# Performance work log

Hardware: AMD Instinct MI355X
Metric: run time of the kernel (lower is better)

Reference implementation:

```python
import jax, jax.numpy as jnp
import numpy as np

B, T, F = 512, 512, 16
UNITS = [64, 32, 32, 32]
VOCAB, EDIM = 1281, 4


def setup_inputs() -> dict:
    key = jax.random.key(0)
    ks = jax.random.split(key, 32)
    x = jax.random.normal(ks[0], (B, T, F), jnp.float32)
    # column 1 holds integer org ids (stored as float, as in the TF model)
    ids = jax.random.randint(ks[1], (B, T), 0, VOCAB).astype(jnp.float32)
    x = x.at[:, :, 1].set(ids)
    d = {"input_tensor": x,
         "emb": jax.random.normal(ks[2], (VOCAB, EDIM), jnp.float32) * 0.05}
    din = 1 + (F - 2) + EDIM  # 18
    i = 3
    for l, u in enumerate(UNITS):
        d[f"k{l}"] = jax.random.normal(ks[i], (din, 3 * u), jnp.float32) * 0.1; i += 1
        d[f"r{l}"] = jax.random.normal(ks[i], (u, 3 * u), jnp.float32) * 0.1; i += 1
        d[f"bi{l}"] = jnp.zeros((3 * u,), jnp.float32)
        d[f"bh{l}"] = jnp.zeros((3 * u,), jnp.float32)
        din = u
    u = UNITS[-1]
    d["w1"] = jax.random.normal(ks[i], (u, u), jnp.float32) * 0.1; i += 1
    d["b1"] = jnp.zeros((u,), jnp.float32)
    d["w2"] = jax.random.normal(ks[i], (u, u), jnp.float32) * 0.1; i += 1
    d["b2"] = jnp.zeros((u,), jnp.float32)
    d["v"] = jax.random.normal(ks[i], (u, 1), jnp.float32) * 0.1; i += 1
    d["bv"] = jnp.zeros((1,), jnp.float32)
    d["wd"] = jax.random.normal(ks[i], (u, 2), jnp.float32) * 0.1; i += 1
    d["bd"] = jnp.zeros((2,), jnp.float32)
    return d


def _gru(h, xp, rk, bh):
    # Keras GRUCell (reset_after=True). xp = x @ kernel + input_bias, [B, 3u]
    hp = h @ rk + bh
    xz, xr, xh = jnp.split(xp, 3, axis=-1)
    hz, hr, hhp = jnp.split(hp, 3, axis=-1)
    z = jax.nn.sigmoid(xz + hz)
    r = jax.nn.sigmoid(xr + hr)
    hh = jnp.tanh(xh + r * hhp)
    return z * h + (1.0 - z) * hh


def _forward(input_tensor, emb, k0, r0, bi0, bh0, k1, r1, bi1, bh1,
             k2, r2, bi2, bh2, k3, r3, bi3, bh3,
             w1, b1, w2, b2, v, bv, wd, bd):
    f0 = input_tensor[:, :, :1]                      # [B,T,1]
    ids = input_tensor[:, :, 1].astype(jnp.int32)    # [B,T]
    rest = input_tensor[:, :, 2:]                    # [B,T,F-2]
    e = emb[ids]                                     # [B,T,4]
    inp = jnp.concatenate([f0, rest, e], axis=2)     # [B,T,din]

    # precompute layer-0 input projection as one big GEMM
    xp0 = inp @ k0 + bi0                             # [B,T,3*64]
    bsz = inp.shape[0]
    init = tuple(jnp.zeros((bsz, u), inp.dtype) for u in UNITS)

    def step(carry, xp_t):
        h0, h1, h2, h3 = carry
        h0 = _gru(h0, xp_t, r0, bh0)
        h1 = _gru(h1, h0 @ k1 + bi1, r1, bh1)
        h2 = _gru(h2, h1 @ k2 + bi2, r2, bh2)
        h3 = _gru(h3, h2 @ k3 + bi3, r3, bh3)
        return (h0, h1, h2, h3), h3

    (_, _, _, hT), seq = jax.lax.scan(step, init, jnp.swapaxes(xp0, 0, 1))
    outputs = jnp.swapaxes(seq, 0, 1)                # [B,T,32] (last-layer sequence)

    # Bahdanau attention: query = final state of last layer
    score = jnp.tanh(outputs @ w1 + b1 + (hT @ w2 + b2)[:, None, :]) @ v + bv  # [B,T,1]
    attn = jax.nn.softmax(score, axis=1)
    ctx = jnp.sum(attn * outputs, axis=1)            # [B,32]
    return jax.nn.softmax(ctx @ wd + bd, axis=-1)    # [B,2]


def reference(input_tensor, emb, k0, r0, bi0, bh0, k1, r1, bi1, bh1,
              k2, r2, bi2, bh2, k3, r3, bi3, bh3,
              w1, b1, w2, b2, v, bv, wd, bd):
    return _forward(input_tensor, emb, k0, r0, bi0, bh0, k1, r1, bi1, bh1,
                    k2, r2, bi2, bh2, k3, r3, bi3, bh3,
                    w1, b1, w2, b2, v, bv, wd, bd)
```

## Files before the change

kernel.cpp:

```cpp
#include <hip/hip_runtime.h>

#define TLEN 512
#define FIN 16

__device__ __forceinline__ float sigm(float x) { return 1.0f / (1.0f + __expf(-x)); }
__device__ __forceinline__ float tanh_f(float x) {
  x = fminf(fmaxf(x, -15.0f), 15.0f);
  float e = __expf(2.0f * x);
  return (e - 1.0f) / (e + 1.0f);
}

__device__ __forceinline__ float gru_fin(float own_main, float own_xh, float own_hhp,
                                         int role, float hold) {
  const float oth_main = __shfl_xor(own_main, 1);
  const float xh  = own_xh  + __shfl_xor(own_xh, 1);
  const float hhp = own_hhp + __shfl_xor(own_hhp, 1);
  const float sz = role ? oth_main : own_main;
  const float sr = role ? own_main : oth_main;
  const float z = sigm(sz);
  const float r = sigm(sr);
  const float hh = tanh_f(xh + r * hhp);
  return z * hold + (1.f - z) * hh;
}

__global__ __launch_bounds__(256, 1)
void rnn_pipe2(const float* __restrict__ x, const float* __restrict__ emb,
               const float* __restrict__ k0, const float* __restrict__ r0,
               const float* __restrict__ bi0, const float* __restrict__ bh0,
               const float* __restrict__ k1, const float* __restrict__ r1,
               const float* __restrict__ bi1, const float* __restrict__ bh1,
               const float* __restrict__ k2, const float* __restrict__ r2,
               const float* __restrict__ bi2, const float* __restrict__ bh2,
               const float* __restrict__ k3, const float* __restrict__ r3,
               const float* __restrict__ bi3, const float* __restrict__ bh3,
               const float* __restrict__ w1, const float* __restrict__ b1,
               const float* __restrict__ w2, const float* __restrict__ b2,
               const float* __restrict__ vv, const float* __restrict__ bv,
               const float* __restrict__ wd, const float* __restrict__ bd,
               float* __restrict__ out, float* __restrict__ obuf)
{
  __shared__ __align__(16) float s_h0[2][64][2];
  __shared__ __align__(16) float s_h1[2][32][2];
  __shared__ __align__(16) float s_h2[2][32][2];
  __shared__ __align__(16) float s_h3[2][32][2];
  __shared__ __align__(16) float s_inp[2][20][2];
  __shared__ __align__(16) float s_emb[2][TLEN][4];
  __shared__ __align__(16) float s_pA[2][64][2];
  __shared__ __align__(16) float s_pAh[2][64][2];
  __shared__ __align__(16) float e_w1[1024];
  __shared__ __align__(16) float e_sc[1024];
  __shared__ float e_hw2[64], e_b1[32], e_v[32], e_ctx[64];

  const int tid  = threadIdx.x;
  const int wid  = tid >> 6;
  const int lane = tid & 63;
  const int g    = lane >> 1;
  const int role = lane & 1;
  const int bb0  = blockIdx.x * 2;

  float Wa[96], Wb[48], Wc[48];
  float bm = 0.f, bxh = 0.f, bhh = 0.f;
  float cbm = 0.f, cbxh = 0.f, cbhh = 0.f;
  float rxP = 0.f;

  if (wid <= 1) {
    const int u  = wid * 32 + g;
    const int cm = role ? 64 + u : u;
    #pragma unroll
    for (int j = 0; j < 19; ++j) Wa[j] = k0[j*192 + cm];
    Wa[19] = 0.f;
    #pragma unroll
    for (int j = 0; j < 64; ++j) Wa[20+j] = r0[j*192 + cm];
    #pragma unroll
    for (int jj = 0; jj < 10; ++jj) {
      const int row = role*10 + jj;
      Wb[jj] = (row < 19) ? k0[row*192 + 128 + u] : 0.f;
    }
    #pragma unroll
    for (int jj = 0; jj < 32; ++jj) Wb[10+jj] = r0[(role*32+jj)*192 + 128 + u];
    bm  = bi0[cm] + bh0[cm];
    bxh = role ? 0.f : bi0[128+u];
    bhh = role ? bh0[128+u] : 0.f;
  }
  if (wid == 0) {
    const int cma = role ? 32 + g : g;
    #pragma unroll
    for (int j = 0; j < 32; ++j) Wc[j] = k3[j*96 + cma];
    #pragma unroll
    for (int jj = 0; jj < 16; ++jj) Wc[32+jj] = k3[(role*16+jj)*96 + 64 + g];
  }
  if (wid == 2) {
    const int cm = role ? 32 + g : g;
    #pragma unroll
    for (int j = 0; j < 64; ++j) Wa[j] = k1[j*96 + cm];
    #pragma unroll
    for (int j = 0; j < 32; ++j) Wa[64+j] = r1[j*96 + cm];
    #pragma unroll
    for (int jj = 0; jj < 32; ++jj) Wb[jj] = k1[(role*32+jj)*96 + 64 + g];
    #pragma unroll
    for (int jj = 0; jj < 16; ++jj) Wb[32+jj] = r1[(role*16+jj)*96 + 64 + g];
    bm  = bi1[cm] + bh1[cm];
    bxh = role ? 0.f : bi1[64+g];
    bhh = role ? bh1[64+g] : 0.f;
  }
  if (wid == 3) {
    const int cm = role ? 32 + g : g;
    #pragma unroll
    for (int j = 0; j < 32; ++j) Wa[j] = k2[j*96 + cm];
    #pragma unroll
    for (int j = 0; j < 32; ++j) Wa[32+j] = r2[j*96 + cm];
    #pragma unroll
    for (int jj = 0; jj < 16; ++jj) Wb[jj] = k2[(role*16+jj)*96 + 64 + g];
    #pragma unroll
    for (int jj = 0; jj < 16; ++jj) Wb[16+jj] = r2[(role*16+jj)*96 + 64 + g];
    bm  = bi2[cm] + bh2[cm];
    bxh = role ? 0.f : bi2[64+g];
    bhh = role ? bh2[64+g] : 0.f;
    #pragma unroll
    for (int j = 0; j < 32; ++j) Wc[j] = r3[j*96 + cm];
    #pragma unroll
    for (int jj = 0; jj < 16; ++jj) Wc[32+jj] = r3[(role*16+jj)*96 + 64 + g];
    cbm  = bi3[cm] + bh3[cm];
    cbxh = bi3[64+g];
    cbhh = bh3[64+g];
  }

  ((float*)s_h0)[tid] = 0.f;
  if (tid < 128) {
    ((float*)s_h1)[tid] = 0.f;
    ((float*)s_h2)[tid] = 0.f;
    ((float*)s_h3)[tid] = 0.f;
  }
  if (tid < 80) ((float*)s_inp)[tid] = 0.f;

  for (int q = tid; q < 2*TLEN; q += 256) {
    const int b2 = q >> 9, t2 = q & 511;
    const int id = (int)x[((size_t)(bb0+b2)*TLEN + t2)*FIN + 1];
    *(float4*)&s_emb[b2][t2][0] = *(const float4*)&emb[id*4];
  }
  if (wid == 1 && lane < 32) {
    const int b2 = lane >> 4, f = lane & 15;
    rxP = x[((size_t)(bb0+b2)*TLEN + 1)*FIN + f];
  }
  __syncthreads();
  if (tid < 32) {
    const int b2 = tid >> 4, f = tid & 15;
    const float v = x[((size_t)(bb0+b2)*TLEN + 0)*FIN + f];
    if (f == 0) s_inp[0][0][b2] = v;
    else if (f >= 2) s_inp[0][f-1][b2] = v;
    if (f < 4) s_inp[0][15+f][b2] = s_emb[b2][0][f];
  }

  for (int i = 0; i < 516; ++i) {
    __syncthreads();
    const int wp = i & 1;
    const int rp = wp ^ 1;

    if (wid <= 1) {
      if (i < 512) {
        const int u = wid*32 + g;
        float a0A = bm, a0B = bm, a1A = 0.f, a1B = 0.f;
        #pragma unroll
        for (int j = 0; j < 20; j += 2) {
          const float4 q = *(const float4*)&s_inp[wp][j][0];
          a0A += Wa[j]*q.x;   a0B += Wa[j]*q.y;
          a1A += Wa[j+1]*q.z; a1B += Wa[j+1]*q.w;
        }
        #pragma unroll
        for (int j = 0; j < 64; j += 2) {
          const float4 q = *(const float4*)&s_h0[rp][j][0];
          a0A += Wa[20+j]*q.x; a0B += Wa[20+j]*q.y;
          a1A += Wa[21+j]*q.z; a1B += Wa[21+j]*q.w;
        }
        float xqA = bxh, xqB = bxh;
        #pragma unroll
        for (int jj = 0; jj < 10; ++jj) {
          const float2 d = *(const float2*)&s_inp[wp][role*10+jj][0];
          xqA += Wb[jj]*d.x; xqB += Wb[jj]*d.y;
        }
        float p0A = bhh, p0B = bhh, p1A = 0.f, p1B = 0.f;
        #pragma unroll
        for (int jj = 0; jj < 32; jj += 2) {
          const float4 q = *(const float4*)&s_h0[rp][role*32+jj][0];
          p0A += Wb[10+jj]*q.x; p0B += Wb[10+jj]*q.y;
          p1A += Wb[11+jj]*q.z; p1B += Wb[11+jj]*q.w;
        }
        const float holdA = s_h0[rp][u][0];
        const float holdB = s_h0[rp][u][1];
        const float hnA = gru_fin(a0A+a1A, xqA, p0A+p1A, role, holdA);
        const float hnB = gru_fin(a0B+a1B, xqB, p0B+p1B, role, holdB);
        if (!role) { s_h0[wp][u][0] = hnA; s_h0[wp][u][1] = hnB; }
      }
      if (wid == 0) {
        if (i >= 3 && i <= 514) {
          float q0A=0.f,q0B=0.f,q1A=0.f,q1B=0.f;
          #pragma unroll
          for (int j = 0; j < 32; j += 2) {
            const float4 q = *(const float4*)&s_h2[rp][j][0];
            q0A += Wc[j]*q.x;   q0B += Wc[j]*q.y;
            q1A += Wc[j+1]*q.z; q1B += Wc[j+1]*q.w;
          }
          float phA=0.f, phB=0.f, ph1A=0.f, ph1B=0.f;
          #pragma unroll
          for (int jj = 0; jj < 16; jj += 2) {
            const float4 q = *(const float4*)&s_h2[rp][role*16+jj][0];
            phA  += Wc[32+jj]*q.x; phB  += Wc[32+jj]*q.y;
            ph1A += Wc[33+jj]*q.z; ph1B += Wc[33+jj]*q.w;
          }
          s_pA[wp][lane][0]  = q0A+q1A;  s_pA[wp][lane][1]  = q0B+q1B;
          s_pAh[wp][lane][0] = phA+ph1A; s_pAh[wp][lane][1] = phB+ph1B;
        }
      } else {
        if (lane < 32) {
          const int b2 = lane >> 4, f = lane & 15;
          if (i + 1 <= 511) {
            const int slot = (i+1)&1;
            const float v = rxP;
            if (f == 0) s_inp[slot][0][b2] = v;
            else if (f >= 2) s_inp[slot][f-1][b2] = v;
            if (f < 4) s_inp[slot][15+f][b2] = s_emb[b2][i+1][f];
          }
          if (i + 2 <= 511) rxP = x[((size_t)(bb0+b2)*TLEN + (i+2))*FIN + f];
        }
      }
    } else if (wid == 2) {
      if (i >= 1 && i <= 512) {
        float a0A = bm, a0B = bm, a1A=0.f, a1B=0.f;
        #pragma unroll
        for (int j = 0; j < 64; j += 2) {
          const float4 q = *(const float4*)&s_h0[rp][j][0];
          a0A += Wa[j]*q.x;   a0B += Wa[j]*q.y;
          a1A += Wa[j+1]*q.z; a1B += Wa[j+1]*q.w;
        }
        #pragma unroll
        for (int j = 0; j < 32; j += 2) {
          const float4 q = *(const float4*)&s_h1[rp][j][0];
          a0A += Wa[64+j]*q.x; a0B += Wa[64+j]*q.y;
          a1A += Wa[65+j]*q.z; a1B += Wa[65+j]*q.w;
        }
        float x0A = bxh, x0B = bxh, x1A = 0.f, x1B = 0.f;
        #pragma unroll
        for (int jj = 0; jj < 32; jj += 2) {
          const float4 q = *(const float4*)&s_h0[rp][role*32+jj][0];
          x0A += Wb[jj]*q.x;   x0B += Wb[jj]*q.y;
          x1A += Wb[jj+1]*q.z; x1B += Wb[jj+1]*q.w;
        }
        float p0A = bhh, p0B = bhh, p1A = 0.f, p1B = 0.f;
        #pragma unroll
        for (int jj = 0; jj < 16; jj += 2) {
          const float4 q = *(const float4*)&s_h1[rp][role*16+jj][0];
          p0A += Wb[32+jj]*q.x; p0B += Wb[32+jj]*q.y;
          p1A += Wb[33+jj]*q.z; p1B += Wb[33+jj]*q.w;
        }
        const float holdA = s_h1[rp][g][0];
        const float holdB = s_h1[rp][g][1];
        const float hnA = gru_fin(a0A+a1A, x0A+x1A, p0A+p1A, role, holdA);
        const float hnB = gru_fin(a0B+a1B, x0B+x1B, p0B+p1B, role, holdB);
        if (!role) { s_h1[wp][g][0] = hnA; s_h1[wp][g][1] = hnB; }
      }
    } else {
      if (i >= 2 && i <= 513) {
        float a0A = bm, a0B = bm, a1A=0.f, a1B=0.f;
        #pragma unroll
        for (int j = 0; j < 32; j += 2) {
          const float4 q = *(const float4*)&s_h1[rp][j][0];
          a0A += Wa[j]*q.x;   a0B += Wa[j]*q.y;
          a1A += Wa[j+1]*q.z; a1B += Wa[j+1]*q.w;
        }
        #pragma unroll
        for (int j = 0; j < 32; j += 2) {
          const float4 q = *(const float4*)&s_h2[rp][j][0];
          a0A += Wa[32+j]*q.x; a0B += Wa[32+j]*q.y;
          a1A += Wa[33+j]*q.z; a1B += Wa[33+j]*q.w;
        }
        float x0A = bxh, x0B = bxh, x1A = 0.f, x1B = 0.f;
        #pragma unroll
        for (int jj = 0; jj < 16; jj += 2) {
          const float4 q = *(const float4*)&s_h1[rp][role*16+jj][0];
          x0A += Wb[jj]*q.x;   x0B += Wb[jj]*q.y;
          x1A += Wb[jj+1]*q.z; x1B += Wb[jj+1]*q.w;
        }
        float p0A = bhh, p0B = bhh, p1A = 0.f, p1B = 0.f;
        #pragma unroll
        for (int jj = 0; jj < 16; jj += 2) {
          const float4 q = *(const float4*)&s_h2[rp][role*16+jj][0];
          p0A += Wb[16+jj]*q.x; p0B += Wb[16+jj]*q.y;
          p1A += Wb[17+jj]*q.z; p1B += Wb[17+jj]*q.w;
        }
        const float holdA = s_h2[rp][g][0];
        const float holdB = s_h2[rp][g][1];
        const float hnA = gru_fin(a0A+a1A, x0A+x1A, p0A+p1A, role, holdA);
        const float hnB = gru_fin(a0B+a1B, x0B+x1B, p0B+p1B, role, holdB);
        if (!role) { s_h2[wp][g][0] = hnA; s_h2[wp][g][1] = hnB; }
      }
      if (i >= 4) {
        float q0A=0.f,q0B=0.f,q1A=0.f,q1B=0.f;
        #pragma unroll
        for (int jj = 0; jj < 32; jj += 2) {
          const float4 q = *(const float4*)&s_h3[rp][jj][0];
          q0A += Wc[jj]*q.x;   q0B += Wc[jj]*q.y;
          q1A += Wc[jj+1]*q.z; q1B += Wc[jj+1]*q.w;
        }
        float ph0A=0.f, ph0B=0.f, ph1A=0.f, ph1B=0.f;
        #pragma unroll
        for (int jj = 0; jj < 16; jj += 2) {
          const float4 q = *(const float4*)&s_h3[rp][role*16+jj][0];
          ph0A += Wc[32+jj]*q.x; ph0B += Wc[32+jj]*q.y;
          ph1A += Wc[33+jj]*q.z; ph1B += Wc[33+jj]*q.w;
        }
        const float mainA = s_pA[rp][lane][0] + q0A + q1A + cbm;
        const float mainB = s_pA[rp][lane][1] + q0B + q1B + cbm;
        const float xhA_own = s_pAh[rp][lane][0];
        const float xhB_own = s_pAh[rp][lane][1];
        const float phA_own = ph0A + ph1A;
        const float phB_own = ph0B + ph1B;

        const float othA = __shfl_xor(mainA, 1);
        const float othB = __shfl_xor(mainB, 1);
        const float xhA = xhA_own + __shfl_xor(xhA_own, 1) + cbxh;
        const float xhB = xhB_own + __shfl_xor(xhB_own, 1) + cbxh;
        const float hhpA = phA_own + __shfl_xor(phA_own, 1) + cbhh;
        const float hhpB = phB_own + __shfl_xor(phB_own, 1) + cbhh;

        const float szA = role ? othA : mainA;
        const float srA = role ? mainA : othA;
        const float szB = role ? othB : mainB;
        const float srB = role ? mainB : othB;
        const float zA = sigm(szA), rA = sigm(srA);
        const float zB = sigm(szB), rB = sigm(srB);
        const float hhA = tanh_f(xhA + rA*hhpA);
        const float hhB = tanh_f(xhB + rB*hhpB);
        const float hnA = zA*s_h3[rp][g][0] + (1.f-zA)*hhA;
        const float hnB = zB*s_h3[rp][g][1] + (1.f-zB)*hhB;
        if (!role) {
          s_h3[wp][g][0] = hnA;
          s_h3[wp][g][1] = hnB;
          obuf[((size_t)(bb0+0)*TLEN + (i-4))*32 + g] = hnA;
          obuf[((size_t)(bb0+1)*TLEN + (i-4))*32 + g] = hnB;
        }
      }
    }
  }
  __syncthreads();

  for (int kk = tid; kk < 1024; kk += 256) e_w1[kk] = w1[kk];
  if (tid < 32) { e_b1[tid] = b1[tid]; e_v[tid] = vv[tid]; }
  if (tid >= 64 && tid < 128) {
    const int u = tid & 31, bb = (tid - 64) >> 5;
    float s = b2[u];
    #pragma unroll
    for (int j = 0; j < 32; ++j) s += s_h3[1][j][bb] * w2[j*32 + u];
    e_hw2[bb*32 + u] = s;
  }
  __syncthreads();

  #pragma unroll
  for (int c = 0; c < 4; ++c) {
    const int idx = c*256 + tid;
    const int bb = idx >> 9, t2 = idx & 511;
    const float* row = obuf + ((size_t)(bb0+bb)*TLEN + t2)*32;
    float rr[32];
    #pragma unroll
    for (int j = 0; j < 32; j += 4) {
      const float4 r4 = *(const float4*)&row[j];
      rr[j]=r4.x; rr[j+1]=r4.y; rr[j+2]=r4.z; rr[j+3]=r4.w;
    }
    float sc = 0.f;
    for (int u = 0; u < 32; ++u) {
      float qv = e_b1[u] + e_hw2[bb*32 + u];
      #pragma unroll
      for (int j = 0; j < 32; ++j) qv += rr[j]*e_w1[j*32+u];
      sc += tanh_f(qv)*e_v[u];
    }
    e_sc[idx] = sc;
  }
  __syncthreads();

  {
    if (wid < 2) {
      const int bb = wid;
      float sv[8]; float m = -1e30f;
      #pragma unroll
      for (int k = 0; k < 8; ++k) { sv[k] = e_sc[bb*512 + lane + 64*k]; m = fmaxf(m, sv[k]); }
      #pragma unroll
      for (int off = 32; off > 0; off >>= 1) m = fmaxf(m, __shfl_xor(m, off));
      float ss = 0.f;
      #pragma unroll
      for (int k = 0; k < 8; ++k) { sv[k] = __expf(sv[k]-m); ss += sv[k]; }
      #pragma unroll
      for (int off = 32; off > 0; off >>= 1) ss += __shfl_xor(ss, off);
      const float inv = 1.f/ss;
      #pragma unroll
      for (int k = 0; k < 8; ++k) e_sc[bb*512 + lane + 64*k] = sv[k]*inv;
    }
  }
  __syncthreads();

  if (tid < 64) {
    const int u = tid & 31, bb = tid >> 5;
    float acc = 0.f;
    const float* orow = obuf + (size_t)(bb0+bb)*TLEN*32 + u;
    const float* prow = e_sc + bb*512;
    #pragma unroll 4
    for (int t2 = 0; t2 < 512; ++t2) acc += prow[t2]*orow[(size_t)t2*32];
    e_ctx[bb*32 + u] = acc;
  }
  __syncthreads();

  if (tid < 2) {
    const int bb = tid;
    float l0 = bd[0], l1 = bd[1];
    #pragma unroll
    for (int u = 0; u < 32; ++u) {
      const float cv = e_ctx[bb*32 + u];
      l0 += cv*wd[u*2]; l1 += cv*wd[u*2+1];
    }
    const float mm = fmaxf(l0, l1);
    const float ex0 = __expf(l0-mm), ex1 = __expf(l1-mm);
    const float den = ex0 + ex1;
    out[(bb0+bb)*2 + 0] = ex0/den;
    out[(bb0+bb)*2 + 1] = ex1/den;
  }
}

extern "C" void kernel_launch(void* const* d_in, const int* in_sizes, int n_in,
                              void* d_out, int out_size, void* d_ws, size_t ws_size,
                              hipStream_t stream) {
  const float* x   = (const float*)d_in[0];
  const float* emb = (const float*)d_in[1];
  const float* k0  = (const float*)d_in[2];
  const float* r0  = (const float*)d_in[3];
  const float* bi0 = (const float*)d_in[4];
  const float* bh0 = (const float*)d_in[5];
  const float* k1  = (const float*)d_in[6];
  const float* r1  = (const float*)d_in[7];
  const float* bi1 = (const float*)d_in[8];
  const float* bh1 = (const float*)d_in[9];
  const float* k2  = (const float*)d_in[10];
  const float* r2  = (const float*)d_in[11];
  const float* bi2 = (const float*)d_in[12];
  const float* bh2 = (const float*)d_in[13];
  const float* k3  = (const float*)d_in[14];
  const float* r3  = (const float*)d_in[15];
  const float* bi3 = (const float*)d_in[16];
  const float* bh3 = (const float*)d_in[17];
  const float* w1  = (const float*)d_in[18];
  const float* b1  = (const float*)d_in[19];
  const float* w2  = (const float*)d_in[20];
  const float* b2  = (const float*)d_in[21];
  const float* v   = (const float*)d_in[22];
  const float* bv  = (const float*)d_in[23];
  const float* wd  = (const float*)d_in[24];
  const float* bd  = (const float*)d_in[25];

  float* out  = (float*)d_out;
  float* obuf = (float*)d_ws;

  rnn_pipe2<<<dim3(256), dim3(256), 0, stream>>>(
      x, emb, k0, r0, bi0, bh0, k1, r1, bi1, bh1,
      k2, r2, bi2, bh2, k3, r3, bi3, bh3,
      w1, b1, w2, b2, v, bv, wd, bd, out, obuf);
}
```

Measured before the change: 1.156 ms.

## Preload all timestep inputs into LDS and batch output stores via staging buffer

Instead of a warp prefetching one timestep of input and embedding per iteration into a double-buffered slot, the kernel now loads the whole 512-step input sequence (features plus gathered embedding) into shared memory up front with vectorized loads. Last-layer hidden outputs are staged in a double-buffered shared tile and written to global memory in 16-step chunks as float4 stores by the otherwise idle warp. This takes per-step global loads and scalar global stores off the sequential recurrence critical path. In exchange it uses about 80 KB more LDS and adds a serial prologue before the loop.

After: 1.252 ms. 1.08x slower.

```diff
diff --git a/kernel.cpp b/kernel.cpp
--- a/kernel.cpp
+++ b/kernel.cpp
@@ -24,7 +24,7 @@
 }
 
 __global__ __launch_bounds__(256, 1)
-void rnn_pipe2(const float* __restrict__ x, const float* __restrict__ emb,
+void rnn_pipe3(const float* __restrict__ x, const float* __restrict__ emb,
                const float* __restrict__ k0, const float* __restrict__ r0,
                const float* __restrict__ bi0, const float* __restrict__ bh0,
                const float* __restrict__ k1, const float* __restrict__ r1,
@@ -39,14 +39,14 @@
                const float* __restrict__ wd, const float* __restrict__ bd,
                float* __restrict__ out, float* __restrict__ obuf)
 {
+  __shared__ __align__(16) float s_xin[TLEN][20][2];
   __shared__ __align__(16) float s_h0[2][64][2];
   __shared__ __align__(16) float s_h1[2][32][2];
   __shared__ __align__(16) float s_h2[2][32][2];
   __shared__ __align__(16) float s_h3[2][32][2];
-  __shared__ __align__(16) float s_inp[2][20][2];
-  __shared__ __align__(16) float s_emb[2][TLEN][4];
   __shared__ __align__(16) float s_pA[2][64][2];
   __shared__ __align__(16) float s_pAh[2][64][2];
+  __shared__ __align__(16) float s_fl[2][16][2][32];
   __shared__ __align__(16) float e_w1[1024];
   __shared__ __align__(16) float e_sc[1024];
   __shared__ float e_hw2[64], e_b1[32], e_v[32], e_ctx[64];
@@ -61,7 +61,6 @@
   float Wa[96], Wb[48], Wc[48];
   float bm = 0.f, bxh = 0.f, bhh = 0.f;
   float cbm = 0.f, cbxh = 0.f, cbhh = 0.f;
-  float rxP = 0.f;
 
   if (wid <= 1) {
     const int u  = wid * 32 + g;
@@ -131,25 +130,37 @@
     ((float*)s_h2)[tid] = 0.f;
     ((float*)s_h3)[tid] = 0.f;
   }
-  if (tid < 80) ((float*)s_inp)[tid] = 0.f;
-
-  for (int q = tid; q < 2*TLEN; q += 256) {
-    const int b2 = q >> 9, t2 = q & 511;
-    const int id = (int)x[((size_t)(bb0+b2)*TLEN + t2)*FIN + 1];
-    *(float4*)&s_emb[b2][t2][0] = *(const float4*)&emb[id*4];
-  }
-  if (wid == 1 && lane < 32) {
-    const int b2 = lane >> 4, f = lane & 15;
-    rxP = x[((size_t)(bb0+b2)*TLEN + 1)*FIN + f];
-  }
-  __syncthreads();
-  if (tid < 32) {
-    const int b2 = tid >> 4, f = tid & 15;
-    const float v = x[((size_t)(bb0+b2)*TLEN + 0)*FIN + f];
-    if (f == 0) s_inp[0][0][b2] = v;
-    else if (f >= 2) s_inp[0][f-1][b2] = v;
-    if (f < 4) s_inp[0][15+f][b2] = s_emb[b2][0][f];
-  }
+
+  for (int r = tid; r < 2*TLEN; r += 256) {
+    const int b2 = r & 1, t2 = r >> 1;
+    const float* xr = &x[((size_t)(bb0+b2)*TLEN + t2)*FIN];
+    const float4 x0 = *(const float4*)(xr);
+    const float4 x1 = *(const float4*)(xr+4);
+    const float4 x2 = *(const float4*)(xr+8);
+    const float4 x3 = *(const float4*)(xr+12);
+    float v[20];
+    v[0]=x0.x; v[1]=x0.z; v[2]=x0.w;
+    v[3]=x1.x; v[4]=x1.y; v[5]=x1.z; v[6]=x1.w;
+    v[7]=x2.x; v[8]=x2.y; v[9]=x2.z; v[10]=x2.w;
+    v[11]=x3.x; v[12]=x3.y; v[13]=x3.z; v[14]=x3.w;
+    const int id = (int)x0.y;
+    const float4 e4 = *(const float4*)&emb[id*4];
+    v[15]=e4.x; v[16]=e4.y; v[17]=e4.z; v[18]=e4.w; v[19]=0.f;
+    #pragma unroll
+    for (int j = 0; j < 20; ++j) s_xin[t2][j][b2] = v[j];
+  }
+
+  auto flush = [&](int c) {
+    const int par = c & 1;
+    #pragma unroll
+    for (int it = 0; it < 4; ++it) {
+      const int f4 = it*64 + lane;
+      const int u4 = f4 & 7, row = f4 >> 3;
+      const int dt = row >> 1, b2 = row & 1;
+      const float4 vq = *(const float4*)&s_fl[par][dt][b2][u4*4];
+      *(float4*)&obuf[(((size_t)(bb0+b2)*TLEN) + c*16 + dt)*32 + u4*4] = vq;
+    }
+  };
 
   for (int i = 0; i < 516; ++i) {
     __syncthreads();
@@ -162,7 +173,7 @@
         float a0A = bm, a0B = bm, a1A = 0.f, a1B = 0.f;
         #pragma unroll
         for (int j = 0; j < 20; j += 2) {
-          const float4 q = *(const float4*)&s_inp[wp][j][0];
+          const float4 q = *(const float4*)&s_xin[i][j][0];
           a0A += Wa[j]*q.x;   a0B += Wa[j]*q.y;
           a1A += Wa[j+1]*q.z; a1B += Wa[j+1]*q.w;
         }
@@ -175,7 +186,7 @@
         float xqA = bxh, xqB = bxh;
         #pragma unroll
         for (int jj = 0; jj < 10; ++jj) {
-          const float2 d = *(const float2*)&s_inp[wp][role*10+jj][0];
+          const float2 d = *(const float2*)&s_xin[i][role*10+jj][0];
           xqA += Wb[jj]*d.x; xqB += Wb[jj]*d.y;
         }
         float p0A = bhh, p0B = bhh, p1A = 0.f, p1B = 0.f;
@@ -211,17 +222,7 @@
           s_pAh[wp][lane][0] = phA+ph1A; s_pAh[wp][lane][1] = phB+ph1B;
         }
       } else {
-        if (lane < 32) {
-          const int b2 = lane >> 4, f = lane & 15;
-          if (i + 1 <= 511) {
-            const int slot = (i+1)&1;
-            const float v = rxP;
-            if (f == 0) s_inp[slot][0][b2] = v;
-            else if (f >= 2) s_inp[slot][f-1][b2] = v;
-            if (f < 4) s_inp[slot][15+f][b2] = s_emb[b2][i+1][f];
-          }
-          if (i + 2 <= 511) rxP = x[((size_t)(bb0+b2)*TLEN + (i+2))*FIN + f];
-        }
+        if (i >= 20 && ((i - 20) & 15) == 0) flush((i - 20) >> 4);
       }
     } else if (wid == 2) {
       if (i >= 1 && i <= 512) {
@@ -335,13 +336,16 @@
         if (!role) {
           s_h3[wp][g][0] = hnA;
           s_h3[wp][g][1] = hnB;
-          obuf[((size_t)(bb0+0)*TLEN + (i-4))*32 + g] = hnA;
-          obuf[((size_t)(bb0+1)*TLEN + (i-4))*32 + g] = hnB;
+          const int t3 = i - 4;
+          s_fl[(t3>>4)&1][t3&15][0][g] = hnA;
+          s_fl[(t3>>4)&1][t3&15][1][g] = hnB;
         }
       }
     }
   }
   __syncthreads();
+
+  if (wid == 1) flush(31);
 
   for (int kk = tid; kk < 1024; kk += 256) e_w1[kk] = w1[kk];
   if (tid < 32) { e_b1[tid] = b1[tid]; e_v[tid] = vv[tid]; }
@@ -456,7 +460,7 @@
   float* out  = (float*)d_out;
   float* obuf = (float*)d_ws;
 
-  rnn_pipe2<<<dim3(256), dim3(256), 0, stream>>>(
+  rnn_pipe3<<<dim3(256), dim3(256), 0, stream>>>(
       x, emb, k0, r0, bi0, bh0, k1, r1, bi1, bh1,
       k2, r2, bi2, bh2, k3, r3, bi3, bh3,
       w1, b1, w2, b2, v, bv, wd, bd, out, obuf);
```
